# Optimization experiments

Hardware: AMD Instinct MI355X
Metric: run time of the kernel (lower is better)

The kernel has to match this reference:

```python
import jax, jax.numpy as jnp
import numpy as np

N_NODES = 100000
N_EDGES = 2000000
D = 128
REL_TYPES = 64


def setup_inputs() -> dict:
    key = jax.random.key(0)
    k1, k2, k3, k4 = jax.random.split(key, 4)
    z = jax.random.normal(k1, (N_NODES, D), dtype=jnp.float32)
    edge_index = jax.random.randint(k2, (2, N_EDGES), 0, N_NODES, dtype=jnp.int64)
    rel_id = jax.random.randint(k3, (N_EDGES,), 0, REL_TYPES, dtype=jnp.int64)
    rel = jax.random.normal(k4, (REL_TYPES, D), dtype=jnp.float32)
    return {"z": z, "edge_index": edge_index, "rel_id": rel_id, "rel": rel}


def reference(z, edge_index, rel_id, rel):
    # DistMult: sigmoid(sum_d z[src,d] * rel[rel_id,d] * z[dst,d])
    src = z[edge_index[0]]          # [E, D]
    dst = z[edge_index[1]]          # [E, D]
    r = rel[rel_id]                 # [E, D]
    scores = jnp.sum(src * r * dst, axis=1)  # [E]
    return jax.nn.sigmoid(scores)
```

## Files before the change

### kernel.cpp

```cpp
#include <hip/hip_runtime.h>
#include <hip/hip_fp16.h>
#include <stdint.h>


#define NSRC 8
#define NDST 64
#define NBKT 512
#define CNT_STRIDE 16
#define SC_BLOCKS 512
#define PE 16
#define EPB 128

#if defined(__has_builtin)
#if __has_builtin(__builtin_amdgcn_fdot2)
#define HAS_FDOT2 1
#endif
#endif

typedef _Float16 hv2 __attribute__((ext_vector_type(2)));

__device__ __forceinline__ float dot3_accum(uint32_t a, uint32_t r, uint32_t b,
                                            float acc)
{
#ifdef HAS_FDOT2
    union { uint32_t u; hv2 v; } A, R, B;
    A.u = a; R.u = r; B.u = b;
    const hv2 t = A.v * R.v;
    return __builtin_amdgcn_fdot2(t, B.v, acc, false);
#else
    union { uint32_t u; __half2 h; } A, R, B;
    A.u = a; R.u = r; B.u = b;
    const float2 af = __half22float2(A.h);
    const float2 rf = __half22float2(R.h);
    const float2 bf = __half22float2(B.h);
    acc = fmaf(af.x * rf.x, bf.x, acc);
    acc = fmaf(af.y * rf.y, bf.y, acc);
    return acc;
#endif
}

__global__ __launch_bounds__(256) void convert_kernel(
    const float* __restrict__ x, __half* __restrict__ xh, int n8)
{
    const int i = blockIdx.x * blockDim.x + threadIdx.x;
    if (i >= n8) return;
    const float4 f0 = ((const float4*)x)[2 * i];
    const float4 f1 = ((const float4*)x)[2 * i + 1];
    union { __half2 h2[4]; uint4 u; } o;
    o.h2[0] = __floats2half2_rn(f0.x, f0.y);
    o.h2[1] = __floats2half2_rn(f0.z, f0.w);
    o.h2[2] = __floats2half2_rn(f1.x, f1.y);
    o.h2[3] = __floats2half2_rn(f1.z, f1.w);
    ((uint4*)xh)[i] = o.u;
}

__device__ __forceinline__ uint32_t bucket_of2(uint32_t s, uint32_t d, uint32_t nn) {
    uint32_t ss = (s * (uint32_t)NSRC) / nn; if (ss > NSRC - 1) ss = NSRC - 1;
    uint32_t ds = (d * (uint32_t)NDST) / nn; if (ds > NDST - 1) ds = NDST - 1;
    return ss * NDST + ds;
}

__global__ __launch_bounds__(256) void scatter_reg_kernel(
    const int* __restrict__ src, const int* __restrict__ dst,
    const int* __restrict__ relid, int E, int nn, int cap,
    uint32_t* __restrict__ counters, uint64_t* __restrict__ binned)
{
    __shared__ uint32_t hist[NBKT];
    __shared__ uint32_t cursor[NBKT];

    const int chunk = (E + (int)gridDim.x - 1) / (int)gridDim.x;
    const int lo = blockIdx.x * chunk;
    const int hi = (lo + chunk < E) ? lo + chunk : E;

    for (int t = threadIdx.x; t < NBKT; t += 256) hist[t] = 0;
    __syncthreads();

    uint64_t pay[PE];
    uint32_t bkt[PE];

    #pragma unroll
    for (int p = 0; p < PE; p++) {
        const int i = lo + p * 256 + (int)threadIdx.x;
        if (i < hi) {
            const uint32_t s = (uint32_t)src[i];
            const uint32_t d = (uint32_t)dst[i];
            const uint32_t r = (uint32_t)relid[i];
            const uint32_t b = bucket_of2(s, d, (uint32_t)nn);
            pay[p] = (uint64_t)s | ((uint64_t)d << 17)
                   | ((uint64_t)r << 34) | ((uint64_t)i << 40);
            bkt[p] = b;
            atomicAdd(&hist[b], 1u);
        } else {
            bkt[p] = 0xFFFFFFFFu;
        }
    }
    __syncthreads();

    for (int t = threadIdx.x; t < NBKT; t += 256) {
        const uint32_t c = hist[t];
        cursor[t] = c ? atomicAdd(&counters[t * CNT_STRIDE], c) : 0u;
    }
    __syncthreads();

    #pragma unroll
    for (int p = 0; p < PE; p++) {
        if (bkt[p] != 0xFFFFFFFFu) {
            const uint32_t pos = atomicAdd(&cursor[bkt[p]], 1u);
            if (pos < (uint32_t)cap)
                binned[(size_t)bkt[p] * (size_t)cap + pos] = pay[p];
        }
    }
}

__global__ __launch_bounds__(256) void distmult_bucketed_v3_kernel(
    const __half* __restrict__ zh,
    const uint64_t* __restrict__ binned,
    const uint32_t* __restrict__ counters,
    const __half* __restrict__ relh,
    float* __restrict__ out,
    int cap, int cpb)
{
    const int k     = blockIdx.x & 7;
    const int t     = blockIdx.x >> 3;
    const int j     = t / cpb;
    const int chunk = t - j * cpb;
    const int bkt   = k * NDST + j;

    uint32_t cnt = counters[bkt * CNT_STRIDE];
    if (cnt > (uint32_t)cap) cnt = (uint32_t)cap;
    const uint32_t el_blk = (uint32_t)chunk * (uint32_t)EPB;
    if (el_blk >= cnt) return;

    __shared__ uint4 rel_lds[1024];
    {
        const uint4* rsrc = (const uint4*)relh;
        #pragma unroll
        for (int q = 0; q < 4; q++)
            rel_lds[threadIdx.x + 256 * q] = rsrc[threadIdx.x + 256 * q];
    }
    __syncthreads();

    const int g    = threadIdx.x >> 3;
    const int lane = threadIdx.x & 7;

    const uint64_t* bb = binned + (size_t)bkt * (size_t)cap;
    const uint32_t e_base = el_blk + (uint32_t)g * 4u;

    union U4 { uint4 q; uint32_t w[4]; };
    float acc[4];
    uint32_t eid[4];
    bool valid[4];

    #pragma unroll
    for (int i = 0; i < 4; i++) {
        const uint32_t el = e_base + (uint32_t)i;
        valid[i] = (el < cnt);
        const uint64_t p = bb[valid[i] ? el : 0];
        const uint32_t s = (uint32_t)p & 0x1FFFFu;
        const uint32_t d = (uint32_t)(p >> 17) & 0x1FFFFu;
        const uint32_t r = (uint32_t)(p >> 34) & 0x3Fu;
        eid[i] = (uint32_t)(p >> 40);

        const uint4* sb = (const uint4*)(zh + (size_t)s * 128);
        const uint4* db = (const uint4*)(zh + (size_t)d * 128);
        U4 A0, A1, B0, B1, R0, R1;
        A0.q = sb[lane];
        A1.q = sb[lane + 8];
        B0.q = db[lane];
        B1.q = db[lane + 8];
        R0.q = rel_lds[r * 16 + lane];
        R1.q = rel_lds[r * 16 + lane + 8];

        float a = 0.f;
        #pragma unroll
        for (int q = 0; q < 4; q++) {
            a = dot3_accum(A0.w[q], R0.w[q], B0.w[q], a);
            a = dot3_accum(A1.w[q], R1.w[q], B1.w[q], a);
        }
        acc[i] = a;
    }

    #pragma unroll
    for (int off = 4; off > 0; off >>= 1) {
        #pragma unroll
        for (int i = 0; i < 4; i++)
            acc[i] += __shfl_down(acc[i], off, 8);
    }

    if (lane == 0) {
        #pragma unroll
        for (int i = 0; i < 4; i++)
            if (valid[i])
                out[eid[i]] = 1.0f / (1.0f + __expf(-acc[i]));
    }
}

__global__ __launch_bounds__(256) void distmult_f16_kernel(
    const __half* __restrict__ zh,
    const int* __restrict__ src_idx, const int* __restrict__ dst_idx,
    const int* __restrict__ rel_id, const __half* __restrict__ relh,
    float* __restrict__ out, int E)
{
    const int gtid = blockIdx.x * blockDim.x + threadIdx.x;
    const int g = gtid >> 4;
    const int lane = threadIdx.x & 15;
    const int e0 = g * 2, e1 = e0 + 1;
    if (e0 >= E) return;
    const bool has1 = (e1 < E);

    const int s0 = src_idx[e0], d0 = dst_idx[e0], r0 = rel_id[e0];
    const int s1 = has1 ? src_idx[e1] : s0;
    const int d1 = has1 ? dst_idx[e1] : d0;
    const int r1 = has1 ? rel_id[e1]  : r0;

    union U4 { uint4 q; uint32_t w[4]; };
    U4 A0, B0, A1, B1, R0, R1;
    A0.q = ((const uint4*)(zh + (size_t)s0 * 128))[lane];
    B0.q = ((const uint4*)(zh + (size_t)d0 * 128))[lane];
    A1.q = ((const uint4*)(zh + (size_t)s1 * 128))[lane];
    B1.q = ((const uint4*)(zh + (size_t)d1 * 128))[lane];
    R0.q = ((const uint4*)(relh + (size_t)r0 * 128))[lane];
    R1.q = ((const uint4*)(relh + (size_t)r1 * 128))[lane];

    float v0 = 0.f, v1 = 0.f;
    #pragma unroll
    for (int q = 0; q < 4; q++) {
        v0 = dot3_accum(A0.w[q], R0.w[q], B0.w[q], v0);
        v1 = dot3_accum(A1.w[q], R1.w[q], B1.w[q], v1);
    }
    #pragma unroll
    for (int off = 8; off > 0; off >>= 1) {
        v0 += __shfl_down(v0, off, 16);
        v1 += __shfl_down(v1, off, 16);
    }
    if (lane == 0) {
        const float o0 = 1.0f / (1.0f + __expf(-v0));
        if (has1) {
            const float o1 = 1.0f / (1.0f + __expf(-v1));
            *((float2*)(out + e0)) = make_float2(o0, o1);
        } else {
            out[e0] = o0;
        }
    }
}

__global__ __launch_bounds__(256) void distmult_f32_kernel(
    const float* __restrict__ z,
    const int* __restrict__ src_idx, const int* __restrict__ dst_idx,
    const int* __restrict__ rel_id, const float* __restrict__ rel,
    float* __restrict__ out, int E)
{
    const int gtid = blockIdx.x * blockDim.x + threadIdx.x;
    const int e = gtid >> 4;
    const int lane = threadIdx.x & 15;
    if (e >= E) return;
    const int s = src_idx[e], d = dst_idx[e], r = rel_id[e];
    const float4* zs = (const float4*)(z + (size_t)s * 128);
    const float4* zd = (const float4*)(z + (size_t)d * 128);
    const float4* rr = (const float4*)(rel + (size_t)r * 128);
    const float4 a0 = zs[lane], a1 = zs[lane + 16];
    const float4 b0 = zd[lane], b1 = zd[lane + 16];
    const float4 c0 = rr[lane], c1 = rr[lane + 16];
    float v = a0.x * c0.x * b0.x + a0.y * c0.y * b0.y
            + a0.z * c0.z * b0.z + a0.w * c0.w * b0.w
            + a1.x * c1.x * b1.x + a1.y * c1.y * b1.y
            + a1.z * c1.z * b1.z + a1.w * c1.w * b1.w;
    #pragma unroll
    for (int off = 8; off > 0; off >>= 1) v += __shfl_down(v, off, 16);
    if (lane == 0) out[e] = 1.0f / (1.0f + __expf(-v));
}

extern "C" void kernel_launch(void* const* d_in, const int* in_sizes, int n_in,
                              void* d_out, int out_size, void* d_ws, size_t ws_size,
                              hipStream_t stream) {
    const float* z     = (const float*)d_in[0];
    const int*   eidx  = (const int*)d_in[1];
    const int*   relid = (const int*)d_in[2];
    const float* rel   = (const float*)d_in[3];
    float*       out   = (float*)d_out;

    const int nz   = in_sizes[0];
    const int E    = in_sizes[2];
    const int nrel = in_sizes[3];
    const int nn   = nz / 128;
    const int* src = eidx;
    const int* dst = eidx + E;

    const int mean_b = E / NBKT;
    int cap = mean_b + E / 8192 + 512;
    cap = (cap + EPB - 1) & ~(EPB - 1);
    const int cpb = cap / EPB;

    const int sc_blocks = ((E + PE * 256 - 1) / (PE * 256) > SC_BLOCKS)
                        ? (E + PE * 256 - 1) / (PE * 256) : SC_BLOCKS;

    const size_t sz_zh    = (size_t)nz * sizeof(__half);
    const size_t off_rh   = (sz_zh + 255) & ~(size_t)255;
    const size_t sz_rh    = (size_t)nrel * sizeof(__half);
    const size_t off_cnt  = (off_rh + sz_rh + 255) & ~(size_t)255;
    const size_t sz_cnt   = (size_t)NBKT * CNT_STRIDE * 4;
    const size_t off_bin  = (off_cnt + sz_cnt + 255) & ~(size_t)255;
    const size_t sz_bin   = (size_t)NBKT * (size_t)cap * 8;
    const size_t need     = off_bin + sz_bin;

    const bool rel_ok  = (nrel == 64 * 128);
    const bool bits_ok = (nn <= 131072) && (E <= (1 << 21)) && (nz % 8 == 0);

    if (ws_size >= need && rel_ok && bits_ok) {
        char* ws = (char*)d_ws;
        __half*   zh       = (__half*)(ws);
        __half*   rh       = (__half*)(ws + off_rh);
        uint32_t* counters = (uint32_t*)(ws + off_cnt);
        uint64_t* binned   = (uint64_t*)(ws + off_bin);

        const int n8z = nz / 8, n8r = nrel / 8;
        convert_kernel<<<(n8z + 255) / 256, 256, 0, stream>>>(z, zh, n8z);
        convert_kernel<<<(n8r + 255) / 256, 256, 0, stream>>>(rel, rh, n8r);
        hipMemsetAsync(counters, 0, sz_cnt, stream);
        scatter_reg_kernel<<<sc_blocks, 256, 0, stream>>>(
            src, dst, relid, E, nn, cap, counters, binned);
        distmult_bucketed_v3_kernel<<<NSRC * NDST * cpb, 256, 0, stream>>>(
            zh, binned, counters, rh, out, cap, cpb);
    } else if (ws_size >= off_rh + sz_rh && rel_ok && nz % 8 == 0) {
        __half* zh = (__half*)d_ws;
        __half* rh = (__half*)((char*)d_ws + off_rh);
        const int n8z = nz / 8, n8r = nrel / 8;
        convert_kernel<<<(n8z + 255) / 256, 256, 0, stream>>>(z, zh, n8z);
        convert_kernel<<<(n8r + 255) / 256, 256, 0, stream>>>(rel, rh, n8r);
        const int groups = (E + 1) / 2;
        const int blocks = (groups * 16 + 255) / 256;
        distmult_f16_kernel<<<blocks, 256, 0, stream>>>(
            zh, src, dst, relid, rh, out, E);
    } else {
        const int blocks = (E * 16 + 255) / 256;
        distmult_f32_kernel<<<blocks, 256, 0, stream>>>(z, src, dst, relid, rel, out, E);
    }
}
```

Measured before the change: 217.5 us.

## Merge conversion and scatter kernels, replicate bucket counters to cut atomic contention

Fuses the z and rel fp32-to-fp16 conversions into the binning/scatter launch as extra blocks, removing two kernel launches and letting conversion overlap with scattering. Each bucket is split into two replicas with separate counters and storage, chosen by block parity, to spread global atomic traffic. PE is halved and the scatter grid is raised to at least 1024 blocks for more parallelism. The compute kernel iterates over replicas, which adds more, smaller blocks and padding waste per sub-bucket, and the smaller per-replica capacity margin raises overflow risk.

```diff
diff --git a/kernel.cpp b/kernel.cpp
--- a/kernel.cpp
+++ b/kernel.cpp
@@ -6,9 +6,9 @@
 #define NSRC 8
 #define NDST 64
 #define NBKT 512
+#define NREP 2
 #define CNT_STRIDE 16
-#define SC_BLOCKS 512
-#define PE 16
+#define PE 8
 #define EPB 128
 
 #if defined(__has_builtin)
@@ -39,11 +39,15 @@
 #endif
 }
 
-__global__ __launch_bounds__(256) void convert_kernel(
-    const float* __restrict__ x, __half* __restrict__ xh, int n8)
-{
-    const int i = blockIdx.x * blockDim.x + threadIdx.x;
-    if (i >= n8) return;
+__device__ __forceinline__ uint32_t bucket_of2(uint32_t s, uint32_t d, uint32_t nn) {
+    uint32_t ss = (s * (uint32_t)NSRC) / nn; if (ss > NSRC - 1) ss = NSRC - 1;
+    uint32_t ds = (d * (uint32_t)NDST) / nn; if (ds > NDST - 1) ds = NDST - 1;
+    return ss * NDST + ds;
+}
+
+__device__ __forceinline__ void convert8(const float* __restrict__ x,
+                                         __half* __restrict__ xh, int i)
+{
     const float4 f0 = ((const float4*)x)[2 * i];
     const float4 f1 = ((const float4*)x)[2 * i + 1];
     union { __half2 h2[4]; uint4 u; } o;
@@ -54,22 +58,33 @@
     ((uint4*)xh)[i] = o.u;
 }
 
-__device__ __forceinline__ uint32_t bucket_of2(uint32_t s, uint32_t d, uint32_t nn) {
-    uint32_t ss = (s * (uint32_t)NSRC) / nn; if (ss > NSRC - 1) ss = NSRC - 1;
-    uint32_t ds = (d * (uint32_t)NDST) / nn; if (ds > NDST - 1) ds = NDST - 1;
-    return ss * NDST + ds;
-}
-
-__global__ __launch_bounds__(256) void scatter_reg_kernel(
+__global__ __launch_bounds__(256) void aux_merged_kernel(
+    const float* __restrict__ z, __half* __restrict__ zh, int n8z,
+    const float* __restrict__ rel, __half* __restrict__ rh, int n8r,
     const int* __restrict__ src, const int* __restrict__ dst,
-    const int* __restrict__ relid, int E, int nn, int cap,
-    uint32_t* __restrict__ counters, uint64_t* __restrict__ binned)
-{
+    const int* __restrict__ relid, int E, int nn, int vcap,
+    uint32_t* __restrict__ counters, uint64_t* __restrict__ binned,
+    int sc_blocks, int zc_blocks)
+{
+    const int bid = blockIdx.x;
+    if (bid >= sc_blocks) {
+        const int cb = bid - sc_blocks;
+        if (cb < zc_blocks) {
+            const int i = cb * 256 + (int)threadIdx.x;
+            if (i < n8z) convert8(z, zh, i);
+        } else {
+            const int i = (cb - zc_blocks) * 256 + (int)threadIdx.x;
+            if (i < n8r) convert8(rel, rh, i);
+        }
+        return;
+    }
+
     __shared__ uint32_t hist[NBKT];
     __shared__ uint32_t cursor[NBKT];
 
-    const int chunk = (E + (int)gridDim.x - 1) / (int)gridDim.x;
-    const int lo = blockIdx.x * chunk;
+    const int rep = bid & (NREP - 1);
+    const int chunk = (E + sc_blocks - 1) / sc_blocks;
+    const int lo = bid * chunk;
     const int hi = (lo + chunk < E) ? lo + chunk : E;
 
     for (int t = threadIdx.x; t < NBKT; t += 256) hist[t] = 0;
@@ -98,7 +113,7 @@
 
     for (int t = threadIdx.x; t < NBKT; t += 256) {
         const uint32_t c = hist[t];
-        cursor[t] = c ? atomicAdd(&counters[t * CNT_STRIDE], c) : 0u;
+        cursor[t] = c ? atomicAdd(&counters[(t * NREP + rep) * CNT_STRIDE], c) : 0u;
     }
     __syncthreads();
 
@@ -106,28 +121,31 @@
     for (int p = 0; p < PE; p++) {
         if (bkt[p] != 0xFFFFFFFFu) {
             const uint32_t pos = atomicAdd(&cursor[bkt[p]], 1u);
-            if (pos < (uint32_t)cap)
-                binned[(size_t)bkt[p] * (size_t)cap + pos] = pay[p];
-        }
-    }
-}
-
-__global__ __launch_bounds__(256) void distmult_bucketed_v3_kernel(
+            if (pos < (uint32_t)vcap)
+                binned[(size_t)(bkt[p] * NREP + rep) * (size_t)vcap + pos] = pay[p];
+        }
+    }
+}
+
+__global__ __launch_bounds__(256) void distmult_bucketed_v4_kernel(
     const __half* __restrict__ zh,
     const uint64_t* __restrict__ binned,
     const uint32_t* __restrict__ counters,
     const __half* __restrict__ relh,
     float* __restrict__ out,
-    int cap, int cpb)
+    int vcap, int vcpb)
 {
     const int k     = blockIdx.x & 7;
     const int t     = blockIdx.x >> 3;
-    const int j     = t / cpb;
-    const int chunk = t - j * cpb;
-    const int bkt   = k * NDST + j;
-
-    uint32_t cnt = counters[bkt * CNT_STRIDE];
-    if (cnt > (uint32_t)cap) cnt = (uint32_t)cap;
+    const int per_j = NREP * vcpb;
+    const int j     = t / per_j;
+    const int rem   = t - j * per_j;
+    const int rep   = rem / vcpb;
+    const int chunk = rem - rep * vcpb;
+    const int v     = (k * NDST + j) * NREP + rep;
+
+    uint32_t cnt = counters[v * CNT_STRIDE];
+    if (cnt > (uint32_t)vcap) cnt = (uint32_t)vcap;
     const uint32_t el_blk = (uint32_t)chunk * (uint32_t)EPB;
     if (el_blk >= cnt) return;
 
@@ -143,7 +161,7 @@
     const int g    = threadIdx.x >> 3;
     const int lane = threadIdx.x & 7;
 
-    const uint64_t* bb = binned + (size_t)bkt * (size_t)cap;
+    const uint64_t* bb = binned + (size_t)v * (size_t)vcap;
     const uint32_t e_base = el_blk + (uint32_t)g * 4u;
 
     union U4 { uint4 q; uint32_t w[4]; };
@@ -193,6 +211,13 @@
             if (valid[i])
                 out[eid[i]] = 1.0f / (1.0f + __expf(-acc[i]));
     }
+}
+
+__global__ __launch_bounds__(256) void convert_kernel(
+    const float* __restrict__ x, __half* __restrict__ xh, int n8)
+{
+    const int i = blockIdx.x * blockDim.x + threadIdx.x;
+    if (i < n8) convert8(x, xh, i);
 }
 
 __global__ __launch_bounds__(256) void distmult_f16_kernel(
@@ -286,21 +311,26 @@
     const int* src = eidx;
     const int* dst = eidx + E;
 
-    const int mean_b = E / NBKT;
-    int cap = mean_b + E / 8192 + 512;
-    cap = (cap + EPB - 1) & ~(EPB - 1);
-    const int cpb = cap / EPB;
-
-    const int sc_blocks = ((E + PE * 256 - 1) / (PE * 256) > SC_BLOCKS)
-                        ? (E + PE * 256 - 1) / (PE * 256) : SC_BLOCKS;
+    const int mean_v = E / (NBKT * NREP);
+    int vcap = mean_v + E / 16384 + 192;
+    vcap = (vcap + EPB - 1) & ~(EPB - 1);
+    const int vcpb = vcap / EPB;
+
+    int sc_blocks = (E + PE * 256 - 1) / (PE * 256);
+    if (sc_blocks < 1024) sc_blocks = 1024;
+    sc_blocks = (sc_blocks + NREP - 1) & ~(NREP - 1);
+
+    const int n8z = nz / 8, n8r = nrel / 8;
+    const int zc_blocks = (n8z + 255) / 256;
+    const int rc_blocks = (n8r + 255) / 256;
 
     const size_t sz_zh    = (size_t)nz * sizeof(__half);
     const size_t off_rh   = (sz_zh + 255) & ~(size_t)255;
     const size_t sz_rh    = (size_t)nrel * sizeof(__half);
     const size_t off_cnt  = (off_rh + sz_rh + 255) & ~(size_t)255;
-    const size_t sz_cnt   = (size_t)NBKT * CNT_STRIDE * 4;
+    const size_t sz_cnt   = (size_t)NBKT * NREP * CNT_STRIDE * 4;
     const size_t off_bin  = (off_cnt + sz_cnt + 255) & ~(size_t)255;
-    const size_t sz_bin   = (size_t)NBKT * (size_t)cap * 8;
+    const size_t sz_bin   = (size_t)NBKT * NREP * (size_t)vcap * 8;
     const size_t need     = off_bin + sz_bin;
 
     const bool rel_ok  = (nrel == 64 * 128);
@@ -313,20 +343,19 @@
         uint32_t* counters = (uint32_t*)(ws + off_cnt);
         uint64_t* binned   = (uint64_t*)(ws + off_bin);
 
-        const int n8z = nz / 8, n8r = nrel / 8;
-        convert_kernel<<<(n8z + 255) / 256, 256, 0, stream>>>(z, zh, n8z);
-        convert_kernel<<<(n8r + 255) / 256, 256, 0, stream>>>(rel, rh, n8r);
         hipMemsetAsync(counters, 0, sz_cnt, stream);
-        scatter_reg_kernel<<<sc_blocks, 256, 0, stream>>>(
-            src, dst, relid, E, nn, cap, counters, binned);
-        distmult_bucketed_v3_kernel<<<NSRC * NDST * cpb, 256, 0, stream>>>(
-            zh, binned, counters, rh, out, cap, cpb);
+        const int aux_grid = sc_blocks + zc_blocks + rc_blocks;
+        aux_merged_kernel<<<aux_grid, 256, 0, stream>>>(
+            z, zh, n8z, rel, rh, n8r,
+            src, dst, relid, E, nn, vcap, counters, binned,
+            sc_blocks, zc_blocks);
+        distmult_bucketed_v4_kernel<<<NSRC * NDST * NREP * vcpb, 256, 0, stream>>>(
+            zh, binned, counters, rh, out, vcap, vcpb);
     } else if (ws_size >= off_rh + sz_rh && rel_ok && nz % 8 == 0) {
         __half* zh = (__half*)d_ws;
         __half* rh = (__half*)((char*)d_ws + off_rh);
-        const int n8z = nz / 8, n8r = nrel / 8;
-        convert_kernel<<<(n8z + 255) / 256, 256, 0, stream>>>(z, zh, n8z);
-        convert_kernel<<<(n8r + 255) / 256, 256, 0, stream>>>(rel, rh, n8r);
+        convert_kernel<<<zc_blocks, 256, 0, stream>>>(z, zh, n8z);
+        convert_kernel<<<rc_blocks, 256, 0, stream>>>(rel, rh, n8r);
         const int groups = (E + 1) / 2;
         const int blocks = (groups * 16 + 255) / 256;
         distmult_f16_kernel<<<blocks, 256, 0, stream>>>(
```

Measured after the change: 216.2 us. Within noise of the previous version (-0.6%).
